# Optimization experiments

Measured on AMD Instinct MI355X. Metric: run time of the kernel, lower is better.

The kernel has to match this reference:

```python
import jax, jax.numpy as jnp
import numpy as np
from jax import lax

N_WIRES = 4
EPS_BN = 1e-5

def _conv(x, w, b):
    y = lax.conv_general_dilated(x, w, (1, 1), 'SAME',
                                 dimension_numbers=('NCHW', 'OIHW', 'NCHW'))
    return y + b[None, :, None, None]

def _bn2d(x, g, b):
    mu = jnp.mean(x, axis=(0, 2, 3), keepdims=True)
    var = jnp.var(x, axis=(0, 2, 3), keepdims=True)
    return (x - mu) * lax.rsqrt(var + EPS_BN) * g[None, :, None, None] + b[None, :, None, None]

def _maxpool2(x):
    return lax.reduce_window(x, -jnp.inf, lax.max, (1, 1, 2, 2), (1, 1, 2, 2), 'VALID')

def _ry(t):
    c, s = jnp.cos(t / 2), jnp.sin(t / 2)
    return jnp.stack([jnp.stack([c, -s], -1), jnp.stack([s, c], -1)], -2).astype(jnp.complex64)

def _rz(t):
    tc = t.astype(jnp.complex64)
    em, ep = jnp.exp(-0.5j * tc), jnp.exp(0.5j * tc)
    z = jnp.zeros_like(em)
    return jnp.stack([jnpp_stack := jnp.stack([em, z], -1), jnp.stack([z, ep], -1)], -2)

def _rx(t):
    c = jnp.cos(t / 2).astype(jnp.complex64)
    s = (-1j) * jnp.sin(t / 2).astype(jnp.complex64)
    return jnp.stack([jnp.stack([c, s], -1), jnp.stack([s, c], -1)], -2)

def _apply_1q(state, U, q):
    # state: (B,2,2,2,2); U: (2,2) shared or (B,2,2) per-sample
    a = jnp.moveaxis(state, 1 + q, 1)
    if U.ndim == 2:
        a = jnp.einsum('ij,bj...->bi...', U, a)
    else:
        a = jnp.einsum('bij,bj...->bi...', U, a)
    return jnp.moveaxis(a, 1, 1 + q)

def _cnot(state, c, t):
    a = jnp.moveaxis(state, (1 + c, 1 + t), (1, 2))
    a = jnp.stack([a[:, 0], jnp.flip(a[:, 1], axis=1)], axis=1)
    return jnp.moveaxis(a, (1, 2), (1 + c, 1 + t))

def _circuit(scaled, theta, rho):
    # scaled: (B, 4) angles; theta, rho: (4, 3)
    B = scaled.shape[0]
    state = jnp.zeros((B,) + (2,) * N_WIRES, jnp.complex64)
    state = state.at[(slice(None),) + (0,) * N_WIRES].set(1.0 + 0j)
    for i in range(N_WIRES):
        state = _apply_1q(state, _ry(scaled[:, i]), i)
    for i in range(N_WIRES):
        state = _apply_1q(state, _ry(theta[i, 0]), i)
        state = _apply_1q(state, _rz(theta[i, 1]), i)
        state = _apply_1q(state, _rx(theta[i, 2]), i)
    for i in range(N_WIRES - 1):
        state = _cnot(state, i, i + 1)
    for i in range(N_WIRES):
        state = _apply_1q(state, _ry(rho[i, 0]), i)
        state = _apply_1q(state, _rz(rho[i, 1]), i)
        state = _apply_1q(state, _rx(rho[i, 2]), i)
    for i in range(N_WIRES - 1):
        state = _cnot(state, i + 1, i)
    probs = jnp.abs(state) ** 2  # (B,2,2,2,2)
    exps = []
    for i in range(N_WIRES):
        p = jnp.moveaxis(probs, 1 + i, 1)
        exps.append(jnp.sum(p[:, 0], axis=(1, 2, 3)) - jnp.sum(p[:, 1], axis=(1, 2, 3)))
    return jnp.stack(exps, axis=1)  # (B,4)

def setup_inputs() -> dict:
    key = jax.random.key(0)
    ks = jax.random.split(key, 8)
    B = 128
    return {
        'x': jax.random.normal(ks[0], (B, 1, 224, 224), jnp.float32),
        'conv1_w': jax.random.normal(ks[1], (8, 1, 3, 3), jnp.float32) * 0.1,
        'conv1_b': jnp.zeros((8,), jnp.float32),
        'bn1_g': jnp.ones((8,), jnp.float32),
        'bn1_b': jnp.zeros((8,), jnp.float32),
        'conv2_w': jax.random.normal(ks[2], (16, 8, 3, 3), jnp.float32) * 0.1,
        'conv2_b': jnp.zeros((16,), jnp.float32),
        'bn2_g': jnp.ones((16,), jnp.float32),
        'bn2_b': jnp.zeros((16,), jnp.float32),
        'theta': jax.random.normal(ks[3], (4, 3), jnp.float32),
        'rho': jax.random.normal(ks[4], (4, 3), jnp.float32),
        'norm_g': jnp.ones((4,), jnp.float32),
        'norm_b': jnp.zeros((4,), jnp.float32),
    }

def reference(x, conv1_w, conv1_b, bn1_g, bn1_b, conv2_w, conv2_b, bn2_g, bn2_b,
              theta, rho, norm_g, norm_b):
    h = jax.nn.relu(_bn2d(_conv(x, conv1_w, conv1_b), bn1_g, bn1_b))
    h = _maxpool2(h)
    h = jax.nn.relu(_bn2d(_conv(h, conv2_w, conv2_b), bn2_g, bn2_b))
    h = _maxpool2(h)
    feat = jnp.mean(h, axis=(2, 3))          # AdaptiveAvgPool2d((1,1)) + flatten -> (B,16)
    feat = feat[:, :N_WIRES]                  # (B,4)
    scaled = (feat - jnp.mean(feat)) / (jnp.std(feat, ddof=1) + 1e-6) * jnp.pi
    out = _circuit(scaled, theta, rho)        # (B,4) real
    mu = jnp.mean(out, axis=0, keepdims=True)
    var = jnp.var(out, axis=0, keepdims=True)
    return (out - mu) * lax.rsqrt(var + EPS_BN) * norm_g[None, :] + norm_b[None, :]
```

## Files before the change

kernel.cpp:

```cpp
#include <hip/hip_runtime.h>
#include <math.h>

#define H1 224
#define W1 224
#define H2 112
#define W2 112
#define HP 56
#define WP 56

#define NS 32
#define SLOT_STRIDE 64

struct C2 { float re, im; };
__device__ __forceinline__ C2 cmul(C2 a, C2 b) {
    return C2{fmaf(a.re, b.re, -a.im * b.im), fmaf(a.re, b.im, a.im * b.re)};
}
__device__ __forceinline__ C2 cadd(C2 a, C2 b) { return C2{a.re + b.re, a.im + b.im}; }

template <int S>
__device__ __forceinline__ void ap1s(C2* st, C2 u00, C2 u01, C2 u10, C2 u11) {
#pragma unroll
    for (int i = 0; i < 16; i++) {
        if (i & S) continue;
        C2 a0 = st[i], a1 = st[i + S];
        st[i]     = cadd(cmul(u00, a0), cmul(u01, a1));
        st[i + S] = cadd(cmul(u10, a0), cmul(u11, a1));
    }
}
template <int SC, int STT>
__device__ __forceinline__ void cnot_s(C2* st) {
#pragma unroll
    for (int i = 0; i < 16; i++)
        if ((i & SC) && !(i & STT)) { C2 t = st[i]; st[i] = st[i + STT]; st[i + STT] = t; }
}
struct M2 { C2 m[2][2]; };
__device__ __forceinline__ M2 mmul(const M2& A, const M2& B) {
    M2 R;
#pragma unroll
    for (int i = 0; i < 2; i++)
#pragma unroll
        for (int j = 0; j < 2; j++)
            R.m[i][j] = cadd(cmul(A.m[i][0], B.m[0][j]), cmul(A.m[i][1], B.m[1][j]));
    return R;
}
__device__ __forceinline__ M2 combined_u(const float* __restrict__ p) {
    float c0 = cosf(0.5f * p[0]), s0 = sinf(0.5f * p[0]);
    float c1 = cosf(0.5f * p[1]), s1 = sinf(0.5f * p[1]);
    float c2 = cosf(0.5f * p[2]), s2 = sinf(0.5f * p[2]);
    M2 Ry = {{{{c0, 0.f}, {-s0, 0.f}}, {{s0, 0.f}, {c0, 0.f}}}};
    M2 Rz = {{{{c1, -s1}, {0.f, 0.f}}, {{0.f, 0.f}, {c1, s1}}}};
    M2 Rx = {{{{c2, 0.f}, {0.f, -s2}}, {{0.f, -s2}, {c2, 0.f}}}};
    return mmul(Rx, mmul(Rz, Ry));
}

template <int Q>
__device__ __forceinline__ void rows_reduce(float* red, const float* vals, int tid) {
#pragma unroll
    for (int q = 0; q < Q; q++) red[q * 256 + tid] = vals[q];
    __syncthreads();
#pragma unroll
    for (int s = 128; s > 0; s >>= 1) {
        for (int idx = tid; idx < Q * s; idx += 256) {
            int row = idx / s, i = idx - row * s;
            red[row * 256 + i] += red[row * 256 + i + s];
        }
        __syncthreads();
    }
}

__global__ void zero_ws(float* ws, int n) {
    int i = blockIdx.x * blockDim.x + threadIdx.x;
    if (i < n) ws[i] = 0.f;
}

__device__ __forceinline__ float slot_sum(const float* stats, int c) {
    float s = 0.f;
#pragma unroll
    for (int sl = 0; sl < NS; sl++) s += stats[sl * SLOT_STRIDE + c];
    return s;
}


__device__ __forceinline__ void conv1_item_body(
        int b, int strip, const float* __restrict__ x, const float* __restrict__ w,
        const float* __restrict__ bias, const bool* gp,
        float* __restrict__ stats1p, float* __restrict__ p1ext,
        float* red, int tid, int witem) {
    int pc = tid & 127;
    int rhalf = tid >> 7;
    int r0 = strip * 16 + rhalf * 8;
    const float* xb = x + (size_t)b * H1 * W1;
    float sums[8], sqs[8], pm[8];
#pragma unroll
    for (int c = 0; c < 8; c++) { sums[c] = 0.f; sqs[c] = 0.f; }
    bool act = pc < W2;
    if (act) {
        bool cl = pc > 0, cr = pc < W2 - 1;
        const float* rp0 = xb + (size_t)r0 * W1 + 2 * pc;
        float al, am0, am1, ar, bl, bm0, bm1, br;
        if (r0 > 0) {
            const float* rp = rp0 - W1;
            float2 m = *(const float2*)rp;
            al = cl ? rp[-1] : 0.f; am0 = m.x; am1 = m.y; ar = cr ? rp[2] : 0.f;
        } else { al = 0.f; am0 = 0.f; am1 = 0.f; ar = 0.f; }
        {
            float2 m = *(const float2*)rp0;
            bl = cl ? rp0[-1] : 0.f; bm0 = m.x; bm1 = m.y; br = cr ? rp0[2] : 0.f;
        }
#pragma unroll
        for (int rr = 0; rr < 8; rr++) {
            float nl = 0.f, nm0 = 0.f, nm1 = 0.f, nr = 0.f;
            int rn = r0 + rr + 1;
            if (rn < H1) {
                const float* rp = rp0 + (size_t)(rr + 1) * W1;
                float2 m = *(const float2*)rp;
                nl = cl ? rp[-1] : 0.f; nm0 = m.x; nm1 = m.y; nr = cr ? rp[2] : 0.f;
            }
            float4 e0 = make_float4(0.f, 0.f, 0.f, 0.f);
            float4 e1 = make_float4(0.f, 0.f, 0.f, 0.f);
#pragma unroll
            for (int c = 0; c < 8; c++) {
                const float* wc = w + c * 9;
                float y0 = bias[c], y1 = bias[c];
                y0 = fmaf(wc[0], al,  y0); y0 = fmaf(wc[1], am0, y0); y0 = fmaf(wc[2], am1, y0);
                y1 = fmaf(wc[0], am0, y1); y1 = fmaf(wc[1], am1, y1); y1 = fmaf(wc[2], ar,  y1);
                y0 = fmaf(wc[3], bl,  y0); y0 = fmaf(wc[4], bm0, y0); y0 = fmaf(wc[5], bm1, y0);
                y1 = fmaf(wc[3], bm0, y1); y1 = fmaf(wc[4], bm1, y1); y1 = fmaf(wc[5], br,  y1);
                y0 = fmaf(wc[6], nl,  y0); y0 = fmaf(wc[7], nm0, y0); y0 = fmaf(wc[8], nm1, y0);
                y1 = fmaf(wc[6], nm0, y1); y1 = fmaf(wc[7], nm1, y1); y1 = fmaf(wc[8], nr,  y1);
                sums[c] += y0 + y1;
                sqs[c] = fmaf(y0, y0, fmaf(y1, y1, sqs[c]));
                float m01 = gp[c] ? fmaxf(y0, y1) : fminf(y0, y1);
                if ((rr & 1) == 0) {
                    pm[c] = m01;
                } else {
                    float e = gp[c] ? fmaxf(pm[c], m01) : fminf(pm[c], m01);
                    if (c == 0) e0.x = e; else if (c == 1) e0.y = e;
                    else if (c == 2) e0.z = e; else if (c == 3) e0.w = e;
                    else if (c == 4) e1.x = e; else if (c == 5) e1.y = e;
                    else if (c == 6) e1.z = e; else e1.w = e;
                }
            }
            if (rr & 1) {
                int pr = (r0 + rr) >> 1;
                float* dst = p1ext + ((((size_t)b * H2 + pr) * W2 + pc) << 3);
                ((float4*)dst)[0] = e0;
                ((float4*)dst)[1] = e1;
            }
            al = bl; am0 = bm0; am1 = bm1; ar = br;
            bl = nl; bm0 = nm0; bm1 = nm1; br = nr;
        }
    }
    float vals[16];
#pragma unroll
    for (int c = 0; c < 8; c++) { vals[c] = sums[c]; vals[8 + c] = sqs[c]; }
    rows_reduce<16>(red, vals, tid);
    if (tid < 16) stats1p[((size_t)witem << 4) + tid] = red[tid * 256];
}

__device__ __forceinline__ void conv2_item_body(
        int b, int Y0, int X0, const float* __restrict__ p1ext,
        const float* sc1, const float* sh1,
        const float* __restrict__ w2, const float* __restrict__ b2,
        const float* __restrict__ g2,
        float* __restrict__ stats2p, float* __restrict__ p2ext,
        float* smem, int tid, int witem) {
    float (*h1t)[34][34] = (float(*)[34][34])smem;
    int ty = tid >> 4, tx = tid & 15;
    const float* pb = p1ext + (((size_t)b * H2) * W2 << 3);
    for (int i = tid; i < 34 * 34; i += 256) {
        int p = i / 34, q = i % 34;
        int hy = Y0 - 1 + p, hx = X0 - 1 + q;
        if (hy >= 0 && hy < H2 && hx >= 0 && hx < W2) {
            const float* cp = pb + (((size_t)hy * W2 + hx) << 3);
            float4 u = ((const float4*)cp)[0];
            float4 v = ((const float4*)cp)[1];
            h1t[0][p][q] = fmaxf(fmaf(u.x, sc1[0], sh1[0]), 0.f);
            h1t[1][p][q] = fmaxf(fmaf(u.y, sc1[1], sh1[1]), 0.f);
            h1t[2][p][q] = fmaxf(fmaf(u.z, sc1[2], sh1[2]), 0.f);
            h1t[3][p][q] = fmaxf(fmaf(u.w, sc1[3], sh1[3]), 0.f);
            h1t[4][p][q] = fmaxf(fmaf(v.x, sc1[4], sh1[4]), 0.f);
            h1t[5][p][q] = fmaxf(fmaf(v.y, sc1[5], sh1[5]), 0.f);
            h1t[6][p][q] = fmaxf(fmaf(v.z, sc1[6], sh1[6]), 0.f);
            h1t[7][p][q] = fmaxf(fmaf(v.w, sc1[7], sh1[7]), 0.f);
        } else {
#pragma unroll
            for (int c = 0; c < 8; c++) h1t[c][p][q] = 0.f;
        }
    }
    __syncthreads();
    float acc[4][2][2];
#pragma unroll
    for (int co = 0; co < 4; co++)
#pragma unroll
        for (int dy = 0; dy < 2; dy++)
#pragma unroll
            for (int dx = 0; dx < 2; dx++) acc[co][dy][dx] = b2[co];
#pragma unroll
    for (int ci = 0; ci < 8; ci++) {
        float win[4][4];
#pragma unroll
        for (int r = 0; r < 4; r++) {
            const float2* rp = (const float2*)&h1t[ci][2 * ty + r][2 * tx];
            float2 u = rp[0], v = rp[1];
            win[r][0] = u.x; win[r][1] = u.y; win[r][2] = v.x; win[r][3] = v.y;
        }
#pragma unroll
        for (int co = 0; co < 4; co++)
#pragma unroll
            for (int ky = 0; ky < 3; ky++)
#pragma unroll
                for (int kx = 0; kx < 3; kx++) {
                    float wv = w2[co * 72 + ci * 9 + ky * 3 + kx];
#pragma unroll
                    for (int dy = 0; dy < 2; dy++)
#pragma unroll
                        for (int dx = 0; dx < 2; dx++)
                            acc[co][dy][dx] = fmaf(wv, win[dy + ky][dx + kx], acc[co][dy][dx]);
                }
    }
    int cy0 = Y0 + 2 * ty, cx0 = X0 + 2 * tx;
    bool vy0 = cy0 < H2, vy1 = cy0 + 1 < H2, vx0 = cx0 < W2, vx1 = cx0 + 1 < W2;
    float vals[8];
#pragma unroll
    for (int co = 0; co < 4; co++) {
        float s = 0.f, q = 0.f;
        if (vy0 && vx0) { float a = acc[co][0][0]; s += a; q = fmaf(a, a, q); }
        if (vy0 && vx1) { float a = acc[co][0][1]; s += a; q = fmaf(a, a, q); }
        if (vy1 && vx0) { float a = acc[co][1][0]; s += a; q = fmaf(a, a, q); }
        if (vy1 && vx1) { float a = acc[co][1][1]; s += a; q = fmaf(a, a, q); }
        vals[co] = s;
        vals[4 + co] = q;
    }
    {
        int hy = (Y0 >> 1) + ty, hx = (X0 >> 1) + tx;
        if (hy < HP && hx < WP) {
#pragma unroll
            for (int co = 0; co < 4; co++) {
                float mx = fmaxf(fmaxf(acc[co][0][0], acc[co][0][1]),
                                 fmaxf(acc[co][1][0], acc[co][1][1]));
                float mn = fminf(fminf(acc[co][0][0], acc[co][0][1]),
                                 fminf(acc[co][1][0], acc[co][1][1]));
                p2ext[(((size_t)b * 4 + co) * HP + hy) * WP + hx] = (g2[co] >= 0.f) ? mx : mn;
            }
        }
    }
    __syncthreads();
    rows_reduce<8>(smem, vals, tid);
    if (tid < 8) stats2p[((size_t)witem << 3) + tid] = smem[tid * 256];
}

__device__ __forceinline__ void pool_item_body(
        int b, int co, const float* __restrict__ p2ext,
        const float* __restrict__ g2, const float* __restrict__ be2,
        const float* __restrict__ stats2p, int nblk2,
        float* __restrict__ featbuf, float N2, float* red, int tid) {
    {
        const float4* sp = (const float4*)stats2p;
        int tot4 = nblk2 << 1;
        float4 a0 = make_float4(0.f, 0.f, 0.f, 0.f);
        float4 a1 = a0;
        int idx = tid;
        for (; idx + 256 < tot4; idx += 512) {
            float4 t0 = sp[idx];
            float4 t1 = sp[idx + 256];
            a0.x += t0.x; a0.y += t0.y; a0.z += t0.z; a0.w += t0.w;
            a1.x += t1.x; a1.y += t1.y; a1.z += t1.z; a1.w += t1.w;
        }
        for (; idx < tot4; idx += 256) {
            float4 t = sp[idx];
            a0.x += t.x; a0.y += t.y; a0.z += t.z; a0.w += t.w;
        }
        a0.x += a1.x; a0.y += a1.y; a0.z += a1.z; a0.w += a1.w;
        ((float4*)red)[tid] = a0;
    }
    __syncthreads();
    if (tid < 8) {
        int hi = tid >> 2, lo = tid & 3;
        float s = 0.f;
#pragma unroll
        for (int k = 0; k < 128; k++) s += red[((hi + (k << 1)) << 2) + lo];
        red[1024 + tid] = s;
    }
    __syncthreads();
    float su = red[1024 + co], sq = red[1024 + 4 + co];
    float mu = su / N2;
    float var = sq / N2 - mu * mu;
    float sc = g2[co] * rsqrtf(var + 1e-5f);
    float sh = be2[co] - mu * sc;
    const float4* P4 = (const float4*)(p2ext + ((size_t)b * 4 + co) * (HP * WP));
    float s = 0.f;
    for (int i = tid; i < (HP * WP) / 4; i += 256) {
        float4 t = P4[i];
        s += fmaxf(fmaf(t.x, sc, sh), 0.f) + fmaxf(fmaf(t.y, sc, sh), 0.f) +
             fmaxf(fmaf(t.z, sc, sh), 0.f) + fmaxf(fmaf(t.w, sc, sh), 0.f);
    }
    __syncthreads();
    red[tid] = s;
    __syncthreads();
    for (int st = 128; st > 0; st >>= 1) {
        if (tid < st) red[tid] += red[tid + st];
        __syncthreads();
    }
    if (tid == 0) atomicExch(featbuf + ((size_t)b * 4 + co), red[0]);
}

__device__ __forceinline__ float bsum(float v, float* lds) {
#pragma unroll
    for (int off = 32; off; off >>= 1) v += __shfl_xor(v, off, 64);
    __syncthreads();
    if ((threadIdx.x & 63) == 0) lds[threadIdx.x >> 6] = v;
    __syncthreads();
    float r = 0.f;
    int nw = (int)(blockDim.x + 63) >> 6;
#pragma clang loop unroll(disable)
    for (int i = 0; i < nw; i++) r += lds[i];
    return r;
}

__device__ __forceinline__ void finalize_body(
        const float* __restrict__ featbuf, const float* __restrict__ theta,
        const float* __restrict__ rho, const float* __restrict__ ng,
        const float* __restrict__ nb, float* __restrict__ out, int B, float* lds) {
    int b = threadIdx.x;
    bool act = b < B;
    float f[4];
#pragma unroll
    for (int j = 0; j < 4; j++) f[j] = act ? featbuf[b * 4 + j] * (1.f / (HP * WP)) : 0.f;
    float n = 4.f * (float)B;
    float mean = bsum(f[0] + f[1] + f[2] + f[3], lds) / n;
    float d2 = 0.f;
    if (act) {
#pragma unroll
        for (int j = 0; j < 4; j++) { float d = f[j] - mean; d2 += d * d; }
    }
    float var1 = bsum(d2, lds) / (n - 1.f);
    float stdv = sqrtf(fmaxf(var1, 0.f)) + 1e-6f;
    const float PI = 3.14159265358979323846f;
    float cs[4], sn[4];
#pragma unroll
    for (int j = 0; j < 4; j++) {
        float sc = (f[j] - mean) / stdv * PI;
        cs[j] = cosf(0.5f * sc);
        sn[j] = sinf(0.5f * sc);
    }
    C2 st[16];
    {
        float amp[16];
        amp[1] = sn[3]; amp[0] = cs[3];
#pragma unroll
        for (int k = 0; k < 2; k++) { amp[k + 2] = amp[k] * sn[2]; amp[k] *= cs[2]; }
#pragma unroll
        for (int k = 0; k < 4; k++) { amp[k + 4] = amp[k] * sn[1]; amp[k] *= cs[1]; }
#pragma unroll
        for (int k = 0; k < 8; k++) { amp[k + 8] = amp[k] * sn[0]; amp[k] *= cs[0]; }
#pragma unroll
        for (int i = 0; i < 16; i++) st[i] = C2{amp[i], 0.f};
    }
#pragma clang loop unroll(disable)
    for (int l = 0; l < 2; l++) {
        const float* p = (l == 0) ? theta : rho;
#pragma clang loop unroll(disable)
        for (int i = 0; i < 4; i++) {
            M2 U = combined_u(p + i * 3);
            switch (i) {
            case 0: ap1s<8>(st, U.m[0][0], U.m[0][1], U.m[1][0], U.m[1][1]); break;
            case 1: ap1s<4>(st, U.m[0][0], U.m[0][1], U.m[1][0], U.m[1][1]); break;
            case 2: ap1s<2>(st, U.m[0][0], U.m[0][1], U.m[1][0], U.m[1][1]); break;
            default: ap1s<1>(st, U.m[0][0], U.m[0][1], U.m[1][0], U.m[1][1]); break;
            }
        }
        if (l == 0) { cnot_s<8, 4>(st); cnot_s<4, 2>(st); cnot_s<2, 1>(st); }
        else        { cnot_s<4, 8>(st); cnot_s<2, 4>(st); cnot_s<1, 2>(st); }
    }
    float e[4];
#pragma unroll
    for (int qb = 0; qb < 4; qb++) {
        int m = 8 >> qb;
        float p0 = 0.f, p1 = 0.f;
#pragma unroll
        for (int i = 0; i < 16; i++) {
            float pr = st[i].re * st[i].re + st[i].im * st[i].im;
            if (i & m) p1 += pr; else p0 += pr;
        }
        e[qb] = p0 - p1;
    }
#pragma clang loop unroll(disable)
    for (int j = 0; j < 4; j++) {
        float mu = bsum(act ? e[j] : 0.f, lds) / (float)B;
        float dv = e[j] - mu;
        float v = bsum(act ? dv * dv : 0.f, lds) / (float)B;
        if (act) out[b * 4 + j] = fmaf(dv, rsqrtf(v + 1e-5f) * ng[j], nb[j]);
    }
}


__global__ __launch_bounds__(256, 2) void conv1_pool_stats(
        const float* __restrict__ x, const float* __restrict__ w,
        const float* __restrict__ bias, const float* __restrict__ g1,
        float* __restrict__ stats1p, float* __restrict__ p1ext) {
    __shared__ float red[16 * 256];
    int strip = blockIdx.x;
    int b = blockIdx.y;
    int tid = threadIdx.x;
    bool gp[8];
#pragma unroll
    for (int c = 0; c < 8; c++) gp[c] = g1[c] >= 0.f;
    conv1_item_body(b, strip, x, w, bias, gp, stats1p, p1ext, red, tid, b * 14 + strip);
}

__global__ __launch_bounds__(256, 4) void conv2_stats_slim(
        const float* __restrict__ p1ext, const float* __restrict__ g1,
        const float* __restrict__ be1, const float* __restrict__ stats1p, int nblk1,
        const float* __restrict__ w2, const float* __restrict__ b2,
        const float* __restrict__ g2,
        float* __restrict__ stats2p, float* __restrict__ p2ext,
        int* __restrict__ cnt, float N1) {
    __shared__ __align__(16) float smem[8 * 34 * 34];
    __shared__ float sc1[8], sh1[8];
    int b = blockIdx.z;
    int tid = threadIdx.y * 16 + threadIdx.x;
    if (tid == 0 && blockIdx.x == 0 && blockIdx.y == 0 && blockIdx.z == 0)
        atomicExch(cnt, 0);
    {
        float* scr = smem;
        const float4* sp = (const float4*)stats1p;
        int tot4 = nblk1 << 2;
        float4 a0 = make_float4(0.f, 0.f, 0.f, 0.f);
        float4 a1 = a0, a2 = a0, a3 = a0;
        int idx = tid;
        for (; idx + 768 < tot4; idx += 1024) {
            float4 t0 = sp[idx];
            float4 t1 = sp[idx + 256];
            float4 t2 = sp[idx + 512];
            float4 t3 = sp[idx + 768];
            a0.x += t0.x; a0.y += t0.y; a0.z += t0.z; a0.w += t0.w;
            a1.x += t1.x; a1.y += t1.y; a1.z += t1.z; a1.w += t1.w;
            a2.x += t2.x; a2.y += t2.y; a2.z += t2.z; a2.w += t2.w;
            a3.x += t3.x; a3.y += t3.y; a3.z += t3.z; a3.w += t3.w;
        }
        for (; idx < tot4; idx += 256) {
            float4 t = sp[idx];
            a0.x += t.x; a0.y += t.y; a0.z += t.z; a0.w += t.w;
        }
        a0.x += a1.x + a2.x + a3.x;
        a0.y += a1.y + a2.y + a3.y;
        a0.z += a1.z + a2.z + a3.z;
        a0.w += a1.w + a2.w + a3.w;
        ((float4*)scr)[tid] = a0;
        __syncthreads();
        if (tid < 16) {
            int hi = tid >> 2, lo = tid & 3;
            float s = 0.f;
#pragma unroll
            for (int k = 0; k < 64; k++) s += scr[((hi + (k << 2)) << 2) + lo];
            scr[1024 + tid] = s;
        }
        __syncthreads();
        if (tid < 8) {
            float su = scr[1024 + tid], sq = scr[1024 + 8 + tid];
            float mu = su / N1;
            float var = sq / N1 - mu * mu;
            float sc = g1[tid] * rsqrtf(var + 1e-5f);
            sc1[tid] = sc;
            sh1[tid] = be1[tid] - mu * sc;
        }
        __syncthreads();
    }
    int blkid = (blockIdx.z * gridDim.y + blockIdx.y) * gridDim.x + blockIdx.x;
    conv2_item_body(b, blockIdx.y * 32, blockIdx.x * 32, p1ext, sc1, sh1,
                    w2, b2, g2, stats2p, p2ext, smem, tid, blkid);
}

__global__ void pool_bn_fin(const float* __restrict__ p2ext,
                            const float* __restrict__ g2, const float* __restrict__ be2,
                            const float* __restrict__ stats2p, int nblk2,
                            float* __restrict__ featbuf,
                            const float* __restrict__ theta, const float* __restrict__ rho,
                            const float* __restrict__ ng, const float* __restrict__ nb,
                            float* __restrict__ out, int B, int* __restrict__ cnt,
                            float N2) {
    __shared__ float red[1024 + 16];
    __shared__ int lastf;
    int tid = threadIdx.x;
    pool_item_body(blockIdx.x >> 2, blockIdx.x & 3, p2ext, g2, be2, stats2p, nblk2,
                   featbuf, N2, red, tid);
    if (tid == 0) {
        __threadfence();
        int old = atomicAdd(cnt, 1);
        lastf = (old == (int)gridDim.x - 1);
    }
    __syncthreads();
    if (lastf) {
        __threadfence();
        finalize_body(featbuf, theta, rho, ng, nb, out, B, red);
    }
}


__global__ void conv1_stats(const float* __restrict__ x, const float* __restrict__ w,
                            const float* __restrict__ bias, float* __restrict__ stats) {
    __shared__ float red[16 * 256];
    int strip = blockIdx.x;
    int b = blockIdx.y;
    int tid = threadIdx.x;
    const float* xb = x + (size_t)b * H1 * W1;
    float sums[8], sqs[8];
#pragma unroll
    for (int c = 0; c < 8; c++) { sums[c] = 0.f; sqs[c] = 0.f; }
    int col = tid;
    if (col < W1) {
        bool cl = col > 0, cr = col < W1 - 1;
        int row0 = strip * 8;
        float a0, a1, a2, b0, b1, b2, c0, c1, c2;
        {
            int r = row0 - 1;
            if (r >= 0) {
                a0 = cl ? xb[r * W1 + col - 1] : 0.f;
                a1 = xb[r * W1 + col];
                a2 = cr ? xb[r * W1 + col + 1] : 0.f;
            } else { a0 = a1 = a2 = 0.f; }
            r = row0;
            b0 = cl ? xb[r * W1 + col - 1] : 0.f;
            b1 = xb[r * W1 + col];
            b2 = cr ? xb[r * W1 + col + 1] : 0.f;
        }
        for (int rr = 0; rr < 8; rr++) {
            int rn = row0 + rr + 1;
            if (rn < H1) {
                c0 = cl ? xb[rn * W1 + col - 1] : 0.f;
                c1 = xb[rn * W1 + col];
                c2 = cr ? xb[rn * W1 + col + 1] : 0.f;
            } else { c0 = c1 = c2 = 0.f; }
#pragma unroll
            for (int c = 0; c < 8; c++) {
                float acc = bias[c];
                acc = fmaf(w[c * 9 + 0], a0, acc);
                acc = fmaf(w[c * 9 + 1], a1, acc);
                acc = fmaf(w[c * 9 + 2], a2, acc);
                acc = fmaf(w[c * 9 + 3], b0, acc);
                acc = fmaf(w[c * 9 + 4], b1, acc);
                acc = fmaf(w[c * 9 + 5], b2, acc);
                acc = fmaf(w[c * 9 + 6], c0, acc);
                acc = fmaf(w[c * 9 + 7], c1, acc);
                acc = fmaf(w[c * 9 + 8], c2, acc);
                sums[c] += acc;
                sqs[c] = fmaf(acc, acc, sqs[c]);
            }
            a0 = b0; a1 = b1; a2 = b2;
            b0 = c0; b1 = c1; b2 = c2;
        }
    }
    float vals[16];
#pragma unroll
    for (int c = 0; c < 8; c++) { vals[c] = sums[c]; vals[8 + c] = sqs[c]; }
    rows_reduce<16>(red, vals, tid);
    int slot = (b * 28 + strip) & (NS - 1);
    if (tid < 16) atomicAdd(stats + slot * SLOT_STRIDE + tid, red[tid * 256]);
}

template <int PH, int PW>
__device__ __forceinline__ void build_h1_tile(const float* __restrict__ xb,
                                              float (*h1t)[PH][PW],
                                              const float* __restrict__ w1,
                                              const float* __restrict__ b1,
                                              const float* sc1, const float* sh1,
                                              int oy0, int ox0, int tid) {
    for (int i = tid; i < PH * PW; i += 256) {
        int p = i / PW, q = i % PW;
        int hy = oy0 + p, hx = ox0 + q;
        bool ok = (hy >= 0 && hy < H2 && hx >= 0 && hx < W2);
        float xp[5][5];
        if (hy >= 1 && hy <= H2 - 2 && hx >= 1 && hx <= W2 - 2) {
            const float* bp = xb + (2 * hy - 1) * W1 + (2 * hx - 1);
#pragma unroll
            for (int r = 0; r < 5; r++)
#pragma unroll
                for (int c = 0; c < 5; c++) xp[r][c] = bp[r * W1 + c];
        } else if (ok) {
#pragma unroll
            for (int r = 0; r < 5; r++)
#pragma unroll
                for (int c = 0; c < 5; c++) {
                    int gy = 2 * hy - 1 + r, gx = 2 * hx - 1 + c;
                    xp[r][c] = (gy >= 0 && gy < H1 && gx >= 0 && gx < W1) ? xb[gy * W1 + gx] : 0.f;
                }
        }
#pragma unroll
        for (int c = 0; c < 8; c++) {
            float mx = 0.f;
            if (ok) {
                mx = -INFINITY;
#pragma unroll
                for (int dy = 0; dy < 2; dy++)
#pragma unroll
                    for (int dx = 0; dx < 2; dx++) {
                        float acc = b1[c];
#pragma unroll
                        for (int ky = 0; ky < 3; ky++)
#pragma unroll
                            for (int kx = 0; kx < 3; kx++)
                                acc = fmaf(w1[c * 9 + ky * 3 + kx], xp[dy + ky][dx + kx], acc);
                        mx = fmaxf(mx, fmaxf(fmaf(acc, sc1[c], sh1[c]), 0.f));
                    }
            }
            h1t[c][p][q] = mx;
        }
    }
}

template <bool STORE>
__global__ __launch_bounds__(256, 4) void conv2_stats_fused(
        const float* __restrict__ x, const float* __restrict__ w1,
        const float* __restrict__ b1, const float* __restrict__ g1,
        const float* __restrict__ be1, const float* __restrict__ stats1,
        const float* __restrict__ w2, const float* __restrict__ b2,
        float* __restrict__ stats2,
        float* __restrict__ pmax, float* __restrict__ pmin, float N1) {
    __shared__ __align__(16) float h1t[8][34][34];
    __shared__ float sc1[8], sh1[8];
    int b = blockIdx.z;
    int Y0 = blockIdx.y * 32, X0 = blockIdx.x * 32;
    int ty = threadIdx.y, tx = threadIdx.x;
    int tid = ty * 16 + tx;
    if (tid < 8) {
        float su = slot_sum(stats1, tid), sq = slot_sum(stats1, 8 + tid);
        float mu = su / N1;
        float var = sq / N1 - mu * mu;
        float sc = g1[tid] * rsqrtf(var + 1e-5f);
        sc1[tid] = sc;
        sh1[tid] = be1[tid] - mu * sc;
    }
    __syncthreads();
    const float* xb = x + (size_t)b * H1 * W1;
    build_h1_tile<34, 34>(xb, h1t, w1, b1, sc1, sh1, Y0 - 1, X0 - 1, tid);
    __syncthreads();
    float acc[4][2][2];
#pragma unroll
    for (int co = 0; co < 4; co++)
#pragma unroll
        for (int dy = 0; dy < 2; dy++)
#pragma unroll
            for (int dx = 0; dx < 2; dx++) acc[co][dy][dx] = b2[co];
#pragma unroll
    for (int ci = 0; ci < 8; ci++) {
        float win[4][4];
#pragma unroll
        for (int r = 0; r < 4; r++) {
            const float2* rp = (const float2*)&h1t[ci][2 * ty + r][2 * tx];
            float2 u = rp[0], v = rp[1];
            win[r][0] = u.x; win[r][1] = u.y; win[r][2] = v.x; win[r][3] = v.y;
        }
#pragma unroll
        for (int co = 0; co < 4; co++)
#pragma unroll
            for (int ky = 0; ky < 3; ky++)
#pragma unroll
                for (int kx = 0; kx < 3; kx++) {
                    float wv = w2[co * 72 + ci * 9 + ky * 3 + kx];
#pragma unroll
                    for (int dy = 0; dy < 2; dy++)
#pragma unroll
                        for (int dx = 0; dx < 2; dx++)
                            acc[co][dy][dx] = fmaf(wv, win[dy + ky][dx + kx], acc[co][dy][dx]);
                }
    }
    int cy0 = Y0 + 2 * ty, cx0 = X0 + 2 * tx;
    bool vy0 = cy0 < H2, vy1 = cy0 + 1 < H2, vx0 = cx0 < W2, vx1 = cx0 + 1 < W2;
    float vals[8];
#pragma unroll
    for (int co = 0; co < 4; co++) {
        float s = 0.f, q = 0.f;
        if (vy0 && vx0) { float a = acc[co][0][0]; s += a; q = fmaf(a, a, q); }
        if (vy0 && vx1) { float a = acc[co][0][1]; s += a; q = fmaf(a, a, q); }
        if (vy1 && vx0) { float a = acc[co][1][0]; s += a; q = fmaf(a, a, q); }
        if (vy1 && vx1) { float a = acc[co][1][1]; s += a; q = fmaf(a, a, q); }
        vals[co] = s;
        vals[4 + co] = q;
    }
    if (STORE) {
        int hy = (Y0 >> 1) + ty, hx = (X0 >> 1) + tx;
        if (hy < HP && hx < WP) {
#pragma unroll
            for (int co = 0; co < 4; co++) {
                float mx = fmaxf(fmaxf(acc[co][0][0], acc[co][0][1]),
                                 fmaxf(acc[co][1][0], acc[co][1][1]));
                float mn = fminf(fminf(acc[co][0][0], acc[co][0][1]),
                                 fminf(acc[co][1][0], acc[co][1][1]));
                size_t idx = (((size_t)b * 4 + co) * HP + hy) * WP + hx;
                pmax[idx] = mx;
                pmin[idx] = mn;
            }
        }
    }
    __syncthreads();
    float* red = (float*)h1t;
    rows_reduce<8>(red, vals, tid);
    int slot = ((b * 16) + blockIdx.y * 4 + blockIdx.x) & (NS - 1);
    if (tid < 8) atomicAdd(stats2 + slot * SLOT_STRIDE + tid, red[tid * 256]);
}

__global__ void pool_bn_mean(const float* __restrict__ pmax, const float* __restrict__ pmin,
                             const float* __restrict__ g2, const float* __restrict__ be2,
                             const float* __restrict__ stats2,
                             float* __restrict__ featbuf, float N2) {
    __shared__ float red[256];
    int co = blockIdx.x & 3;
    int b = blockIdx.x >> 2;
    int tid = threadIdx.x;
    float su = slot_sum(stats2, co), sq = slot_sum(stats2, 4 + co);
    float mu = su / N2;
    float var = sq / N2 - mu * mu;
    float sc = g2[co] * rsqrtf(var + 1e-5f);
    float sh = be2[co] - mu * sc;
    const float* P = (sc >= 0.f ? pmax : pmin) + ((size_t)b * 4 + co) * (HP * WP);
    float s = 0.f;
    for (int i = tid; i < HP * WP; i += 256) s += fmaxf(fmaf(P[i], sc, sh), 0.f);
    red[tid] = s;
    __syncthreads();
    for (int st = 128; st > 0; st >>= 1) {
        if (tid < st) red[tid] += red[tid + st];
        __syncthreads();
    }
    if (tid == 0) featbuf[(size_t)b * 4 + co] = red[0];
}

__global__ void conv2_final_fused(const float* __restrict__ x, const float* __restrict__ w1,
                                  const float* __restrict__ b1, const float* __restrict__ g1,
                                  const float* __restrict__ be1,
                                  const float* __restrict__ stats1,
                                  const float* __restrict__ w2, const float* __restrict__ b2,
                                  const float* __restrict__ g2, const float* __restrict__ be2,
                                  const float* __restrict__ stats2,
                                  float* __restrict__ featbuf, float N1, float N2) {
    __shared__ __align__(16) float h1t[8][34][34];
    __shared__ float sc1[8], sh1[8];
    __shared__ float sc2[4], sh2[4];
    int b = blockIdx.z;
    int py0 = blockIdx.y * 16, px0 = blockIdx.x * 16;
    int ty = threadIdx.y, tx = threadIdx.x;
    int tid = ty * 16 + tx;
    if (tid < 8) {
        float su = slot_sum(stats1, tid), sq = slot_sum(stats1, 8 + tid);
        float mu = su / N1;
        float var = sq / N1 - mu * mu;
        float sc = g1[tid] * rsqrtf(var + 1e-5f);
        sc1[tid] = sc;
        sh1[tid] = be1[tid] - mu * sc;
    }
    if (tid >= 16 && tid < 20) {
        int j = tid - 16;
        float su = slot_sum(stats2, j), sq = slot_sum(stats2, 4 + j);
        float mu = su / N2;
        float var = sq / N2 - mu * mu;
        float sc = g2[j] * rsqrtf(var + 1e-5f);
        sc2[j] = sc;
        sh2[j] = be2[j] - mu * sc;
    }
    __syncthreads();
    const float* xb = x + (size_t)b * H1 * W1;
    build_h1_tile<34, 34>(xb, h1t, w1, b1, sc1, sh1, 2 * py0 - 1, 2 * px0 - 1, tid);
    __syncthreads();
    bool valid = (py0 + ty < HP) && (px0 + tx < WP);
    float acc[4][2][2];
#pragma unroll
    for (int co = 0; co < 4; co++)
#pragma unroll
        for (int dy = 0; dy < 2; dy++)
#pragma unroll
            for (int dx = 0; dx < 2; dx++) acc[co][dy][dx] = b2[co];
#pragma unroll
    for (int ci = 0; ci < 8; ci++) {
        float win[4][4];
#pragma unroll
        for (int r = 0; r < 4; r++) {
            const float2* rp = (const float2*)&h1t[ci][2 * ty + r][2 * tx];
            float2 u = rp[0], v = rp[1];
            win[r][0] = u.x; win[r][1] = u.y; win[r][2] = v.x; win[r][3] = v.y;
        }
#pragma unroll
        for (int co = 0; co < 4; co++)
#pragma unroll
            for (int ky = 0; ky < 3; ky++)
#pragma unroll
                for (int kx = 0; kx < 3; kx++) {
                    float wv = w2[co * 72 + ci * 9 + ky * 3 + kx];
#pragma unroll
                    for (int dy = 0; dy < 2; dy++)
#pragma unroll
                        for (int dx = 0; dx < 2; dx++)
                            acc[co][dy][dx] = fmaf(wv, win[dy + ky][dx + kx], acc[co][dy][dx]);
                }
    }
    float vals[4];
#pragma unroll
    for (int co = 0; co < 4; co++) {
        float mx = -INFINITY;
#pragma unroll
        for (int dy = 0; dy < 2; dy++)
#pragma unroll
            for (int dx = 0; dx < 2; dx++)
                mx = fmaxf(mx, fmaxf(fmaf(acc[co][dy][dx], sc2[co], sh2[co]), 0.f));
        vals[co] = valid ? mx : 0.f;
    }
    __syncthreads();
    float* red = (float*)h1t;
    rows_reduce<4>(red, vals, tid);
    if (tid < 4) atomicAdd(featbuf + (size_t)b * 4 + tid, red[tid * 256]);
}

__global__ void finalize(const float* __restrict__ featbuf, const float* __restrict__ theta,
                         const float* __restrict__ rho, const float* __restrict__ ng,
                         const float* __restrict__ nb, float* __restrict__ out, int B) {
    __shared__ float lds[16];
    finalize_body(featbuf, theta, rho, ng, nb, out, B, lds);
}

extern "C" void kernel_launch(void* const* d_in, const int* in_sizes, int n_in,
                              void* d_out, int out_size, void* d_ws, size_t ws_size,
                              hipStream_t stream) {
    const float* x     = (const float*)d_in[0];
    const float* w1    = (const float*)d_in[1];
    const float* b1    = (const float*)d_in[2];
    const float* g1    = (const float*)d_in[3];
    const float* be1   = (const float*)d_in[4];
    const float* w2    = (const float*)d_in[5];
    const float* b2    = (const float*)d_in[6];
    const float* g2    = (const float*)d_in[7];
    const float* be2   = (const float*)d_in[8];
    const float* theta = (const float*)d_in[9];
    const float* rho   = (const float*)d_in[10];
    const float* ng    = (const float*)d_in[11];
    const float* nb    = (const float*)d_in[12];
    float* out = (float*)d_out;

    int B = in_sizes[0] / (H1 * W1);

    float N1 = (float)B * H1 * W1;
    float N2 = (float)B * H2 * W2;

    int nblk1 = 14 * B;
    int nblk2 = 16 * B;

    size_t p2n = (size_t)B * 4 * HP * WP;
    size_t p1n = (size_t)B * 8 * H2 * W2;

    size_t offs1p = 0;
    size_t offs2p = offs1p + (size_t)nblk1 * 16;
    size_t offfb  = offs2p + (size_t)nblk2 * 8;
    size_t offcnt = offfb + (size_t)B * 4;
    size_t offp2  = offcnt + 4;
    size_t offp1  = offp2 + p2n;
    size_t needA  = (offp1 + p1n) * sizeof(float);

    size_t common = (size_t)(2 * NS * SLOT_STRIDE) + (size_t)B * 4;
    size_t needB = (common + 2 * p2n) * sizeof(float);

    bool tierA = ws_size >= needA;
    bool tierB = !tierA && ws_size >= needB;

    float* ws = (float*)d_ws;

    if (tierA) {
        float* stats1p = ws + offs1p;
        float* stats2p = ws + offs2p;
        float* featbuf = ws + offfb;
        int*   cnt     = (int*)(ws + offcnt);
        float* p2ext   = ws + offp2;
        float* p1ext   = ws + offp1;
        conv1_pool_stats<<<dim3(14, B), 256, 0, stream>>>(x, w1, b1, g1, stats1p, p1ext);
        conv2_stats_slim<<<dim3(4, 4, B), dim3(16, 16), 0, stream>>>(
            p1ext, g1, be1, stats1p, nblk1, w2, b2, g2, stats2p, p2ext, cnt, N1);
        pool_bn_fin<<<B * 4, 256, 0, stream>>>(
            p2ext, g2, be2, stats2p, nblk2, featbuf, theta, rho, ng, nb, out, B, cnt, N2);
    } else if (tierB) {
        float* stats1 = ws;
        float* stats2 = ws + NS * SLOT_STRIDE;
        float* featbuf = ws + 2 * NS * SLOT_STRIDE;
        float* bufs = featbuf + (size_t)B * 4;
        float* pmax = bufs;
        float* pmin = bufs + p2n;
        int nz = (int)common;
        zero_ws<<<(nz + 255) / 256, 256, 0, stream>>>(ws, nz);
        conv1_stats<<<dim3(28, B), 256, 0, stream>>>(x, w1, b1, stats1);
        conv2_stats_fused<true><<<dim3(4, 4, B), dim3(16, 16), 0, stream>>>(
            x, w1, b1, g1, be1, stats1, w2, b2, stats2, pmax, pmin, N1);
        pool_bn_mean<<<B * 4, 256, 0, stream>>>(pmax, pmin, g2, be2, stats2, featbuf, N2);
        finalize<<<1, 256, 0, stream>>>(featbuf, theta, rho, ng, nb, out, B);
    } else {
        float* stats1 = ws;
        float* stats2 = ws + NS * SLOT_STRIDE;
        float* featbuf = ws + 2 * NS * SLOT_STRIDE;
        int nz = (int)common;
        zero_ws<<<(nz + 255) / 256, 256, 0, stream>>>(ws, nz);
        conv1_stats<<<dim3(28, B), 256, 0, stream>>>(x, w1, b1, stats1);
        conv2_stats_fused<false><<<dim3(4, 4, B), dim3(16, 16), 0, stream>>>(
            x, w1, b1, g1, be1, stats1, w2, b2, stats2, nullptr, nullptr, N1);
        conv2_final_fused<<<dim3(4, 4, B), dim3(16, 16), 0, stream>>>(
            x, w1, b1, g1, be1, stats1, w2, b2, g2, be2, stats2, featbuf, N1, N2);
        finalize<<<1, 256, 0, stream>>>(featbuf, theta, rho, ng, nb, out, B);
    }
}
```

Baseline: 182.8 us.

## Split BN1 affine and finalize into separate kernels, drop last-block counter

The BN1 statistics reduction, which every conv2 block repeated redundantly, moves into a single-block affine1 kernel, and conv2 blocks now just load 16 precomputed scale/shift values. The last-block-done atomic counter in the pool kernel is replaced by a separate finalize launch, and the featbuf atomicExch becomes a plain store. This removes repeated global reads of stats1p and atomic/fence traffic, but adds two extra kernel launches and their serialization gaps.

```diff
diff --git a/kernel.cpp b/kernel.cpp
--- a/kernel.cpp
+++ b/kernel.cpp
@@ -302,7 +302,7 @@
         if (tid < st) red[tid] += red[tid + st];
         __syncthreads();
     }
-    if (tid == 0) atomicExch(featbuf + ((size_t)b * 4 + co), red[0]);
+    if (tid == 0) featbuf[(size_t)b * 4 + co] = red[0];
 }
 
 __device__ __forceinline__ float bsum(float v, float* lds) {
@@ -409,92 +409,84 @@
     conv1_item_body(b, strip, x, w, bias, gp, stats1p, p1ext, red, tid, b * 14 + strip);
 }
 
+__global__ void affine1(const float* __restrict__ stats1p, int nblk1,
+                        const float* __restrict__ g1, const float* __restrict__ be1,
+                        float* __restrict__ aff1, float N1) {
+    __shared__ float scr[1024 + 16];
+    int tid = threadIdx.x;
+    const float4* sp = (const float4*)stats1p;
+    int tot4 = nblk1 << 2;
+    float4 a0 = make_float4(0.f, 0.f, 0.f, 0.f);
+    float4 a1 = a0, a2 = a0, a3 = a0;
+    int idx = tid;
+    for (; idx + 768 < tot4; idx += 1024) {
+        float4 t0 = sp[idx];
+        float4 t1 = sp[idx + 256];
+        float4 t2 = sp[idx + 512];
+        float4 t3 = sp[idx + 768];
+        a0.x += t0.x; a0.y += t0.y; a0.z += t0.z; a0.w += t0.w;
+        a1.x += t1.x; a1.y += t1.y; a1.z += t1.z; a1.w += t1.w;
+        a2.x += t2.x; a2.y += t2.y; a2.z += t2.z; a2.w += t2.w;
+        a3.x += t3.x; a3.y += t3.y; a3.z += t3.z; a3.w += t3.w;
+    }
+    for (; idx < tot4; idx += 256) {
+        float4 t = sp[idx];
+        a0.x += t.x; a0.y += t.y; a0.z += t.z; a0.w += t.w;
+    }
+    a0.x += a1.x + a2.x + a3.x;
+    a0.y += a1.y + a2.y + a3.y;
+    a0.z += a1.z + a2.z + a3.z;
+    a0.w += a1.w + a2.w + a3.w;
+    ((float4*)scr)[tid] = a0;
+    __syncthreads();
+    if (tid < 16) {
+        int hi = tid >> 2, lo = tid & 3;
+        float s = 0.f;
+#pragma unroll
+        for (int k = 0; k < 64; k++) s += scr[((hi + (k << 2)) << 2) + lo];
+        scr[1024 + tid] = s;
+    }
+    __syncthreads();
+    if (tid < 8) {
+        float su = scr[1024 + tid], sq = scr[1024 + 8 + tid];
+        float mu = su / N1;
+        float var = sq / N1 - mu * mu;
+        float sc = g1[tid] * rsqrtf(var + 1e-5f);
+        aff1[tid] = sc;
+        aff1[8 + tid] = be1[tid] - mu * sc;
+    }
+}
+
 __global__ __launch_bounds__(256, 4) void conv2_stats_slim(
-        const float* __restrict__ p1ext, const float* __restrict__ g1,
-        const float* __restrict__ be1, const float* __restrict__ stats1p, int nblk1,
+        const float* __restrict__ p1ext, const float* __restrict__ aff1,
         const float* __restrict__ w2, const float* __restrict__ b2,
         const float* __restrict__ g2,
-        float* __restrict__ stats2p, float* __restrict__ p2ext,
-        int* __restrict__ cnt, float N1) {
+        float* __restrict__ stats2p, float* __restrict__ p2ext) {
     __shared__ __align__(16) float smem[8 * 34 * 34];
     __shared__ float sc1[8], sh1[8];
     int b = blockIdx.z;
     int tid = threadIdx.y * 16 + threadIdx.x;
-    if (tid == 0 && blockIdx.x == 0 && blockIdx.y == 0 && blockIdx.z == 0)
-        atomicExch(cnt, 0);
-    {
-        float* scr = smem;
-        const float4* sp = (const float4*)stats1p;
-        int tot4 = nblk1 << 2;
-        float4 a0 = make_float4(0.f, 0.f, 0.f, 0.f);
-        float4 a1 = a0, a2 = a0, a3 = a0;
-        int idx = tid;
-        for (; idx + 768 < tot4; idx += 1024) {
-            float4 t0 = sp[idx];
-            float4 t1 = sp[idx + 256];
-            float4 t2 = sp[idx + 512];
-            float4 t3 = sp[idx + 768];
-            a0.x += t0.x; a0.y += t0.y; a0.z += t0.z; a0.w += t0.w;
-            a1.x += t1.x; a1.y += t1.y; a1.z += t1.z; a1.w += t1.w;
-            a2.x += t2.x; a2.y += t2.y; a2.z += t2.z; a2.w += t2.w;
-            a3.x += t3.x; a3.y += t3.y; a3.z += t3.z; a3.w += t3.w;
-        }
-        for (; idx < tot4; idx += 256) {
-            float4 t = sp[idx];
-            a0.x += t.x; a0.y += t.y; a0.z += t.z; a0.w += t.w;
-        }
-        a0.x += a1.x + a2.x + a3.x;
-        a0.y += a1.y + a2.y + a3.y;
-        a0.z += a1.z + a2.z + a3.z;
-        a0.w += a1.w + a2.w + a3.w;
-        ((float4*)scr)[tid] = a0;
-        __syncthreads();
-        if (tid < 16) {
-            int hi = tid >> 2, lo = tid & 3;
-            float s = 0.f;
-#pragma unroll
-            for (int k = 0; k < 64; k++) s += scr[((hi + (k << 2)) << 2) + lo];
-            scr[1024 + tid] = s;
-        }
-        __syncthreads();
-        if (tid < 8) {
-            float su = scr[1024 + tid], sq = scr[1024 + 8 + tid];
-            float mu = su / N1;
-            float var = sq / N1 - mu * mu;
-            float sc = g1[tid] * rsqrtf(var + 1e-5f);
-            sc1[tid] = sc;
-            sh1[tid] = be1[tid] - mu * sc;
-        }
-        __syncthreads();
-    }
+    if (tid < 8) { sc1[tid] = aff1[tid]; sh1[tid] = aff1[8 + tid]; }
+    __syncthreads();
     int blkid = (blockIdx.z * gridDim.y + blockIdx.y) * gridDim.x + blockIdx.x;
     conv2_item_body(b, blockIdx.y * 32, blockIdx.x * 32, p1ext, sc1, sh1,
                     w2, b2, g2, stats2p, p2ext, smem, tid, blkid);
 }
 
-__global__ void pool_bn_fin(const float* __restrict__ p2ext,
-                            const float* __restrict__ g2, const float* __restrict__ be2,
-                            const float* __restrict__ stats2p, int nblk2,
-                            float* __restrict__ featbuf,
-                            const float* __restrict__ theta, const float* __restrict__ rho,
-                            const float* __restrict__ ng, const float* __restrict__ nb,
-                            float* __restrict__ out, int B, int* __restrict__ cnt,
-                            float N2) {
+__global__ void pool_bn_mean_p(const float* __restrict__ p2ext,
+                               const float* __restrict__ g2, const float* __restrict__ be2,
+                               const float* __restrict__ stats2p, int nblk2,
+                               float* __restrict__ featbuf, float N2) {
     __shared__ float red[1024 + 16];
-    __shared__ int lastf;
-    int tid = threadIdx.x;
     pool_item_body(blockIdx.x >> 2, blockIdx.x & 3, p2ext, g2, be2, stats2p, nblk2,
-                   featbuf, N2, red, tid);
-    if (tid == 0) {
-        __threadfence();
-        int old = atomicAdd(cnt, 1);
-        lastf = (old == (int)gridDim.x - 1);
-    }
-    __syncthreads();
-    if (lastf) {
-        __threadfence();
-        finalize_body(featbuf, theta, rho, ng, nb, out, B, red);
-    }
+                   featbuf, N2, red, threadIdx.x);
+}
+
+__global__ void finalize(const float* __restrict__ featbuf, const float* __restrict__ theta,
+                         const float* __restrict__ rho, const float* __restrict__ ng,
+                         const float* __restrict__ nb, float* __restrict__ out, int B) {
+    __shared__ float lds[16];
+    finalize_body(featbuf, theta, rho, ng, nb, out, B, lds);
 }
 
 
@@ -809,13 +801,6 @@
     if (tid < 4) atomicAdd(featbuf + (size_t)b * 4 + tid, red[tid * 256]);
 }
 
-__global__ void finalize(const float* __restrict__ featbuf, const float* __restrict__ theta,
-                         const float* __restrict__ rho, const float* __restrict__ ng,
-                         const float* __restrict__ nb, float* __restrict__ out, int B) {
-    __shared__ float lds[16];
-    finalize_body(featbuf, theta, rho, ng, nb, out, B, lds);
-}
-
 extern "C" void kernel_launch(void* const* d_in, const int* in_sizes, int n_in,
                               void* d_out, int out_size, void* d_ws, size_t ws_size,
                               hipStream_t stream) {
@@ -847,9 +832,9 @@
 
     size_t offs1p = 0;
     size_t offs2p = offs1p + (size_t)nblk1 * 16;
-    size_t offfb  = offs2p + (size_t)nblk2 * 8;
-    size_t offcnt = offfb + (size_t)B * 4;
-    size_t offp2  = offcnt + 4;
+    size_t offaff = offs2p + (size_t)nblk2 * 8;
+    size_t offfb  = offaff + 16;
+    size_t offp2  = offfb + (size_t)B * 4;
     size_t offp1  = offp2 + p2n;
     size_t needA  = (offp1 + p1n) * sizeof(float);
 
@@ -864,15 +849,16 @@
     if (tierA) {
         float* stats1p = ws + offs1p;
         float* stats2p = ws + offs2p;
+        float* aff1    = ws + offaff;
         float* featbuf = ws + offfb;
-        int*   cnt     = (int*)(ws + offcnt);
         float* p2ext   = ws + offp2;
         float* p1ext   = ws + offp1;
         conv1_pool_stats<<<dim3(14, B), 256, 0, stream>>>(x, w1, b1, g1, stats1p, p1ext);
+        affine1<<<1, 256, 0, stream>>>(stats1p, nblk1, g1, be1, aff1, N1);
         conv2_stats_slim<<<dim3(4, 4, B), dim3(16, 16), 0, stream>>>(
-            p1ext, g1, be1, stats1p, nblk1, w2, b2, g2, stats2p, p2ext, cnt, N1);
-        pool_bn_fin<<<B * 4, 256, 0, stream>>>(
-            p2ext, g2, be2, stats2p, nblk2, featbuf, theta, rho, ng, nb, out, B, cnt, N2);
+            p1ext, aff1, w2, b2, g2, stats2p, p2ext);
+        pool_bn_mean_p<<<B * 4, 256, 0, stream>>>(p2ext, g2, be2, stats2p, nblk2, featbuf, N2);
+        finalize<<<1, 256, 0, stream>>>(featbuf, theta, rho, ng, nb, out, B);
     } else if (tierB) {
         float* stats1 = ws;
         float* stats2 = ws + NS * SLOT_STRIDE;
```

Result: faster. 169.8 us (median of 2 runs) (-7.1%).
